# Optimization experiments

Measured on AMD Instinct MI355X. Metric: run time of the kernel, lower is better.

Reference implementation:

```python
import jax, jax.numpy as jnp
import numpy as np

N = 100000
E = 1600000
NEG_SLOPE_ATTN = 0.2   # DGL GATConv default negative_slope
NEG_SLOPE_ACT = 0.01   # F.leaky_relu default


def gat_conv(x, src, dst, W, al, ar, b):
    """DGL-style GATConv with a single head.
    x: [N, Fin]; W: [Fin, H*Fout]; al, ar: [H, Fout]; b: [H*Fout].
    Returns [N, H, Fout]."""
    H, Fout = al.shape
    h = (x @ W).reshape(-1, H, Fout)                 # [N,H,Fout]
    el = jnp.sum(h * al, axis=-1)                    # [N,H]
    er = jnp.sum(h * ar, axis=-1)                    # [N,H]
    e = jax.nn.leaky_relu(el[src] + er[dst], NEG_SLOPE_ATTN)  # [E,H]
    # edge softmax over incoming edges of each dst node
    m = jax.ops.segment_max(e, dst, num_segments=N)  # [N,H]
    ex = jnp.exp(e - m[dst])                         # [E,H]
    denom = jax.ops.segment_sum(ex, dst, num_segments=N)      # [N,H]
    a = ex / denom[dst]                              # [E,H]
    msg = h[src] * a[:, :, None]                     # [E,H,Fout]
    out = jax.ops.segment_sum(msg, dst, num_segments=N)       # [N,H,Fout]
    return out + b.reshape(1, H, Fout)


def setup_inputs() -> dict:
    key = jax.random.key(0)
    ks = jax.random.split(key, 16)
    features = jax.random.normal(ks[0], (N, 3), dtype=jnp.float32)
    src = jax.random.randint(ks[1], (E,), 0, N)
    dst = jax.random.randint(ks[2], (E,), 0, N)

    def glorot(k, shape):
        fan = shape[0] + shape[-1]
        s = jnp.sqrt(2.0 / fan).astype(jnp.float32)
        return jax.random.normal(k, shape, dtype=jnp.float32) * s

    W1 = glorot(ks[3], (3, 64));   al1 = glorot(ks[4], (1, 64));  ar1 = glorot(ks[5], (1, 64));  b1 = jnp.zeros((64,), jnp.float32)
    W2 = glorot(ks[6], (64, 64));  al2 = glorot(ks[7], (1, 64));  ar2 = glorot(ks[8], (1, 64));  b2 = jnp.zeros((64,), jnp.float32)
    W3 = glorot(ks[9], (64, 3));   al3 = glorot(ks[10], (1, 3));  ar3 = glorot(ks[11], (1, 3));  b3 = jnp.zeros((3,), jnp.float32)
    return {"features": features, "src": src, "dst": dst,
            "W1": W1, "al1": al1, "ar1": ar1, "b1": b1,
            "W2": W2, "al2": al2, "ar2": ar2, "b2": b2,
            "W3": W3, "al3": al3, "ar3": ar3, "b3": b3}


def reference(features, src, dst, W1, al1, ar1, b1, W2, al2, ar2, b2, W3, al3, ar3, b3):
    x = gat_conv(features, src, dst, W1, al1, ar1, b1)      # [N,1,64]
    x = jax.nn.leaky_relu(x, NEG_SLOPE_ACT)
    x = gat_conv(x[:, 0, :], src, dst, W2, al2, ar2, b2)     # [N,1,64]
    x = jax.nn.leaky_relu(x, NEG_SLOPE_ACT)
    x = gat_conv(x[:, 0, :], src, dst, W3, al3, ar3, b3)     # [N,1,3]
    return x[:, 0, :]                                        # [N,3]
```

## Files before the change

### kernel.cpp

```cpp
#include <hip/hip_runtime.h>
#include <hip/hip_fp16.h>
#include <math.h>


#define NEG_BIG (-1e30f)
#define SORT_CAP 6144
#define BSTRIDE 6144
#define CHUNK 8192

__device__ inline float waveSum(float v) {
#pragma unroll
  for (int off = 32; off; off >>= 1) v += __shfl_xor(v, off, 64);
  return v;
}

__device__ inline float halfSum(float v) {
#pragma unroll
  for (int off = 16; off; off >>= 1) v += __shfl_xor(v, off, 64);
  return v;
}

__device__ inline float halfMax(float v) {
#pragma unroll
  for (int off = 16; off; off >>= 1) v = fmaxf(v, __shfl_xor(v, off, 64));
  return v;
}

__device__ inline int waveMaxI(int v) {
#pragma unroll
  for (int off = 32; off; off >>= 1) v = max(v, __shfl_xor(v, off, 64));
  return v;
}

__device__ inline int rlI(int v, int l) { return __builtin_amdgcn_readlane(v, l); }
__device__ inline float rlF(float v, int l) {
  return __int_as_float(__builtin_amdgcn_readlane(__float_as_int(v), l));
}
__device__ inline int ntI(const int* p) { return __builtin_nontemporal_load(p); }

__global__ __launch_bounds__(1024) void k_bin(
    const int* __restrict__ src, const int* __restrict__ dst,
    int* __restrict__ gcursor, unsigned* __restrict__ binned, int E, int NBK) {
  __shared__ int lcnt[512];
  __shared__ int lbase[512];
  int tid = threadIdx.x;
  for (int b = tid; b < NBK; b += 1024) lcnt[b] = 0;
  __syncthreads();
  int e0 = blockIdx.x * CHUNK;
  int e1 = min(e0 + CHUNK, E);
  for (int e = e0 + tid; e < e1; e += 1024)
    atomicAdd(&lcnt[ntI(&dst[e]) >> 8], 1);
  __syncthreads();
  for (int b = tid; b < NBK; b += 1024) {
    int c = lcnt[b];
    lbase[b] = c ? atomicAdd(&gcursor[b], c) : 0;
    lcnt[b] = 0;
  }
  __syncthreads();
  for (int e = e0 + tid; e < e1; e += 1024) {
    int dd = ntI(&dst[e]);
    int ss = ntI(&src[e]);
    int b = dd >> 8;
    int pos = lbase[b] + atomicAdd(&lcnt[b], 1);
    if (pos < BSTRIDE)
      binned[(size_t)b * BSTRIDE + pos] =
          ((unsigned)(dd & 255) << 24) | (unsigned)ss;
  }
}

__global__ __launch_bounds__(256) void k_sort(
    const unsigned* __restrict__ binned, const int* __restrict__ gcount,
    int* __restrict__ csr, int* __restrict__ startv, int N, int E, int NBK) {
  __shared__ unsigned sbuf[SORT_CAP];
  __shared__ unsigned obuf[SORT_CAP];
  __shared__ int hist[256];
  __shared__ int scn[256];
  __shared__ int cur[256];
  __shared__ int sscan[512];
  int b = blockIdx.x;
  int tid = threadIdx.x;
  sscan[tid] = (tid < NBK) ? gcount[tid] : 0;
  sscan[tid + 256] = (tid + 256 < NBK) ? gcount[tid + 256] : 0;
  __syncthreads();
  for (int off = 1; off < 512; off <<= 1) {
    int u0 = (tid >= off) ? sscan[tid - off] : 0;
    int u1 = (tid + 256 >= off) ? sscan[tid + 256 - off] : 0;
    __syncthreads();
    sscan[tid] += u0;
    sscan[tid + 256] += u1;
    __syncthreads();
  }
  int cntb = gcount[b];
  int gbase = sscan[b] - cntb;
  int cnt = min(cntb, BSTRIDE);
  if (b == 0 && tid == 0) startv[N] = E;
  const unsigned* bsrc = binned + (size_t)b * BSTRIDE;
  hist[tid] = 0;
  __syncthreads();
  if (cnt <= SORT_CAP) {
    for (int i = tid; i < cnt; i += 256) {
      unsigned w = bsrc[i];
      sbuf[i] = w;
      atomicAdd(&hist[w >> 24], 1);
    }
    __syncthreads();
    int v = hist[tid];
    scn[tid] = v;
    __syncthreads();
    for (int off = 1; off < 256; off <<= 1) {
      int u = (tid >= off) ? scn[tid - off] : 0;
      __syncthreads();
      scn[tid] += u;
      __syncthreads();
    }
    int excl = scn[tid] - v;
    cur[tid] = excl;
    int dn = b * 256 + tid;
    if (dn < N) startv[dn] = gbase + excl;
    __syncthreads();
    for (int i = tid; i < cnt; i += 256) {
      unsigned w = sbuf[i];
      int p = atomicAdd(&cur[w >> 24], 1);
      obuf[p] = w & 0xFFFFFFu;
    }
    __syncthreads();
    for (int i = tid; i < cnt; i += 256) csr[gbase + i] = (int)obuf[i];
  } else {
    for (int i = tid; i < cnt; i += 256)
      atomicAdd(&hist[bsrc[i] >> 24], 1);
    __syncthreads();
    int v = hist[tid];
    scn[tid] = v;
    __syncthreads();
    for (int off = 1; off < 256; off <<= 1) {
      int u = (tid >= off) ? scn[tid - off] : 0;
      __syncthreads();
      scn[tid] += u;
      __syncthreads();
    }
    int excl = scn[tid] - v;
    cur[tid] = excl;
    int dn = b * 256 + tid;
    if (dn < N) startv[dn] = gbase + excl;
    __syncthreads();
    for (int i = tid; i < cnt; i += 256) {
      unsigned w = bsrc[i];
      int p = atomicAdd(&cur[w >> 24], 1);
      csr[gbase + p] = (int)(w & 0xFFFFFFu);
    }
  }
}

__global__ __launch_bounds__(256) void k_padx(
    const float* __restrict__ x, const float* __restrict__ W1,
    const float* __restrict__ al1, const float* __restrict__ ar1,
    int* __restrict__ gcount, int NBK,
    float4* __restrict__ x4, float* __restrict__ er1, int N) {
  __shared__ float su[6];
  int tid = threadIdx.x;
  if (tid < 64) {
    float a = al1[tid], r = ar1[tid];
#pragma unroll
    for (int i = 0; i < 3; ++i) {
      float w = W1[i * 64 + tid];
      float ui = waveSum(w * a);
      float vi = waveSum(w * r);
      if (tid == 0) { su[i] = ui; su[3 + i] = vi; }
    }
  }
  if (blockIdx.x == 0)
    for (int b = tid; b < NBK; b += 256) gcount[b] = 0;
  __syncthreads();
  int n = blockIdx.x * 256 + tid;
  if (n >= N) return;
  float x0 = __builtin_nontemporal_load(&x[n * 3]);
  float x1 = __builtin_nontemporal_load(&x[n * 3 + 1]);
  float x2 = __builtin_nontemporal_load(&x[n * 3 + 2]);
  float el = fmaf(x0, su[0], fmaf(x1, su[1], x2 * su[2]));
  float er = fmaf(x0, su[3], fmaf(x1, su[4], x2 * su[5]));
  x4[n] = make_float4(x0, x1, x2, el);
  er1[n] = er;
}

__global__ __launch_bounds__(128) void k_agg1x(
    const float4* __restrict__ x4, const float* __restrict__ er1,
    const float* __restrict__ W1, const float* __restrict__ b1,
    const float* __restrict__ W2, const float* __restrict__ al2,
    const float* __restrict__ ar2, const int* __restrict__ start,
    const int* __restrict__ csr, float4* __restrict__ a4,
    float* __restrict__ er2, int N) {
  __shared__ float4 sWp[64];
  __shared__ float2 sLR[64];
  int tid = threadIdx.x;
  if (tid < 64) {
    sWp[tid] = make_float4(W1[tid], W1[64 + tid], W1[128 + tid], b1[tid]);
    float sa = 0.f, sr = 0.f;
#pragma unroll 8
    for (int f = 0; f < 64; ++f) {
      float w = W2[tid * 64 + f];
      sa = fmaf(w, al2[f], sa);
      sr = fmaf(w, ar2[f], sr);
    }
    sLR[tid] = make_float2(sa, sr);
  }
  __syncthreads();
  int n = blockIdx.x * 128 + tid;
  if (n >= N) return;
  int beg = start[n], end = start[n + 1];
  float ern = er1[n];
  float m = NEG_BIG, d = 0.f, X0 = 0.f, X1 = 0.f, X2 = 0.f;
  int s0, s1, s2, s3;
  float4 h0, h1, h2, h3v;
  s0 = (beg + 0 < end) ? ntI(&csr[beg + 0]) : 0;
  s0 = ((unsigned)s0 < (unsigned)N) ? s0 : 0; h0 = x4[s0];
  s1 = (beg + 1 < end) ? ntI(&csr[beg + 1]) : 0;
  s1 = ((unsigned)s1 < (unsigned)N) ? s1 : 0; h1 = x4[s1];
  s2 = (beg + 2 < end) ? ntI(&csr[beg + 2]) : 0;
  s2 = ((unsigned)s2 < (unsigned)N) ? s2 : 0; h2 = x4[s2];
  s3 = (beg + 3 < end) ? ntI(&csr[beg + 3]) : 0;
  s3 = ((unsigned)s3 < (unsigned)N) ? s3 : 0; h3v = x4[s3];
  for (int i = beg; i < end; ++i) {
    float4 hv = h0;
    h0 = h1; h1 = h2; h2 = h3v;
    int ip = i + 4;
    int sp = (ip < end) ? ntI(&csr[ip]) : 0;
    sp = ((unsigned)sp < (unsigned)N) ? sp : 0;
    h3v = x4[sp];
    float e = hv.w + ern;
    e = e > 0.f ? e : 0.2f * e;
    float mn = fmaxf(m, e);
    float sc = __expf(m - mn);
    float q = __expf(e - mn);
    d = fmaf(d, sc, q);
    X0 = fmaf(X0, sc, q * hv.x);
    X1 = fmaf(X1, sc, q * hv.y);
    X2 = fmaf(X2, sc, q * hv.z);
    m = mn;
  }
  float inv = (end > beg) ? 1.f / d : 0.f;
  float A0 = X0 * inv, A1 = X1 * inv, A2 = X2 * inv;
  float el = 0.f, er = 0.f;
#pragma unroll 4
  for (int k = 0; k < 64; ++k) {
    float4 w = sWp[k];
    float v = fmaf(A2, w.z, fmaf(A1, w.y, fmaf(A0, w.x, w.w)));
    v = v > 0.f ? v : 0.01f * v;
    float2 lr = sLR[k];
    el = fmaf(v, lr.x, el);
    er = fmaf(v, lr.y, er);
  }
  a4[n] = make_float4(A0, A1, A2, el);
  er2[n] = er;
}

__global__ __launch_bounds__(64) void k_agg2r(
    const float4* __restrict__ a4, const float* __restrict__ er2,
    const int* __restrict__ start, const int* __restrict__ csr,
    const float* __restrict__ W1, const float* __restrict__ b1,
    __half* __restrict__ xa, int N) {
  __shared__ float4 sAV[64];
  int tid = threadIdx.x;
  int lane = tid & 63, hl = lane & 31, half = lane >> 5;
  int pn = blockIdx.x * 2 + half;
  int n = (pn < N) ? pn : 0;
  int beg = start[n], end = start[n + 1];
  int deg = end - beg;
  int maxd = __builtin_amdgcn_readfirstlane(waveMaxI(deg));
  float ern = er2[n];
  int k0 = 2 * hl;
  float wa0 = W1[k0],     wb0 = W1[64 + k0],     wc0 = W1[128 + k0],     bb0 = b1[k0];
  float wa1 = W1[k0 + 1], wb1 = W1[64 + k0 + 1], wc1 = W1[128 + k0 + 1], bb1 = b1[k0 + 1];
  float acc0 = 0.f, acc1 = 0.f;

  float aA = 0.f, v0s = 0.f, v1s = 0.f, v2s = 0.f;
  if (maxd <= 32) {
    int idx = beg + hl;
    int s = (idx < end) ? ntI(&csr[idx]) : 0;
    s = ((unsigned)s < (unsigned)N) ? s : 0;
    float4 av = a4[s];
    float e = av.w + ern;
    e = e > 0.f ? e : 0.2f * e;
    e = (idx < end) ? e : NEG_BIG;
    float mm = halfMax(e);
    float q = __expf(e - mm);
    float dsum = halfSum(q);
    float inv = (deg > 0) ? 1.f / dsum : 0.f;
    aA = q * inv;
    v0s = av.x; v1s = av.y; v2s = av.z;
  }
  sAV[half * 32 + hl] = make_float4(aA, v0s, v1s, v2s);
  __syncthreads();

  if (maxd <= 32) {
    const float4* sp = &sAV[half * 32];
    for (int j = 0; j < maxd; j += 4) {
#pragma unroll
      for (int k = 0; k < 4; ++k) {
        float4 w = sp[j + k];
        float a = w.x;
        float v0 = fmaf(w.w, wc0, fmaf(w.z, wb0, fmaf(w.y, wa0, bb0)));
        v0 = v0 > 0.f ? v0 : 0.01f * v0;
        float v1 = fmaf(w.w, wc1, fmaf(w.z, wb1, fmaf(w.y, wa1, bb1)));
        v1 = v1 > 0.f ? v1 : 0.01f * v1;
        acc0 = fmaf(a, v0, acc0);
        acc1 = fmaf(a, v1, acc1);
      }
    }
  } else {
    float m = NEG_BIG, dsum = 0.f;
    for (int base = beg; base < end; base += 32) {
      int idx = base + hl;
      int s = (idx < end) ? csr[idx] : 0;
      s = ((unsigned)s < (unsigned)N) ? s : 0;
      float e = a4[s].w + ern;
      e = e > 0.f ? e : 0.2f * e;
      e = (idx < end) ? e : NEG_BIG;
      float mn = fmaxf(m, halfMax(e));
      dsum = dsum * __expf(m - mn) + halfSum(__expf(e - mn));
      m = mn;
    }
    float inv = (deg > 0) ? 1.f / dsum : 0.f;
    for (int base = beg; base < end; base += 32) {
      int idx = base + hl;
      int s = (idx < end) ? csr[idx] : 0;
      s = ((unsigned)s < (unsigned)N) ? s : 0;
      float e = a4[s].w + ern;
      e = e > 0.f ? e : 0.2f * e;
      float a = (idx < end) ? __expf(e - m) * inv : 0.f;
      for (int j = 0; j < 32; ++j) {
        int sAx = rlI(s, j), sBx = rlI(s, j + 32);
        float aAx = rlF(a, j), aBx = rlF(a, j + 32);
        int sj = half ? sBx : sAx;
        float aj = half ? aBx : aAx;
        float4 av = a4[sj];
        float v0 = fmaf(av.z, wc0, fmaf(av.y, wb0, fmaf(av.x, wa0, bb0)));
        v0 = v0 > 0.f ? v0 : 0.01f * v0;
        float v1 = fmaf(av.z, wc1, fmaf(av.y, wb1, fmaf(av.x, wa1, bb1)));
        v1 = v1 > 0.f ? v1 : 0.01f * v1;
        acc0 = fmaf(aj, v0, acc0);
        acc1 = fmaf(aj, v1, acc1);
      }
    }
  }
  if (pn < N) {
    __half2 hv = __float22half2_rn(make_float2(acc0, acc1));
    ((__half2*)xa)[(size_t)pn * 32 + hl] = hv;
  }
}

__global__ __launch_bounds__(256) void k_gemm3(
    const __half* xa_in, const float* __restrict__ W2,
    const float* __restrict__ b2, const float* __restrict__ W3,
    const float* __restrict__ al3, float* __restrict__ h3, int N) {
  __shared__ float sW[64 * 64];
  __shared__ float sX[64 * 64];
  __shared__ float sW3[192];
  int tid = threadIdx.x;
  for (int i = tid; i < 4096; i += 256) sW[i] = W2[i];
  if (tid < 192) sW3[tid] = W3[tid];
  const unsigned* xu = (const unsigned*)xa_in;
  size_t base = (size_t)blockIdx.x * 2048;
  size_t limit = (size_t)N * 32;
  for (int i = tid; i < 2048; i += 256) {
    size_t gi = base + i;
    unsigned u = (gi < limit) ? __builtin_nontemporal_load(&xu[gi]) : 0u;
    __half2 hh = *(__half2*)&u;
    float2 f = __half22float2(hh);
    sX[2 * i] = f.x;
    sX[2 * i + 1] = f.y;
  }
  __syncthreads();
  int wave = tid >> 6, f = tid & 63;
  int r0 = wave * 16;
  float acc[16];
#pragma unroll
  for (int i = 0; i < 16; ++i) acc[i] = 0.f;
  const float2* sX2 = (const float2*)sX;
  for (int k2 = 0; k2 < 32; ++k2) {
    float wv0 = sW[(2 * k2) * 64 + f];
    float wv1 = sW[(2 * k2 + 1) * 64 + f];
#pragma unroll
    for (int i = 0; i < 16; ++i) {
      float2 xv = sX2[(r0 + i) * 32 + k2];
      acc[i] = fmaf(xv.x, wv0, fmaf(xv.y, wv1, acc[i]));
    }
  }
  float bf = b2[f];
  __syncthreads();
#pragma unroll
  for (int i = 0; i < 16; ++i) {
    float r = acc[i] + bf;
    r = r > 0.f ? r : 0.01f * r;
    sX[(r0 + i) * 64 + f] = r;
  }
  __syncthreads();
  int row = tid >> 2, j = tid & 3;
  int j3 = (j < 3) ? j : 0;
  float p = 0.f;
  for (int i = 0; i < 64; ++i) {
    int ff = (row + i) & 63;
    p = fmaf(sX[row * 64 + ff], sW3[ff * 3 + j3], p);
  }
  int lb = (tid & 63) & ~3;
  float q0 = __shfl(p, lb + 0, 64);
  float q1 = __shfl(p, lb + 1, 64);
  float q2 = __shfl(p, lb + 2, 64);
  float val = (j < 3) ? p : fmaf(q0, al3[0], fmaf(q1, al3[1], q2 * al3[2]));
  int grow = blockIdx.x * 64 + row;
  if (grow < N) h3[(size_t)blockIdx.x * 256 + tid] = val;
}

__global__ __launch_bounds__(128) void k_agg3(
    const float4* __restrict__ h3, const int* __restrict__ start,
    const int* __restrict__ csr, const float* __restrict__ ar3,
    const float* __restrict__ b, float* __restrict__ out, int N) {
  int n = blockIdx.x * 128 + threadIdx.x;
  if (n >= N) return;
  int beg = start[n], end = start[n + 1];
  float4 hn = h3[n];
  float ern = fmaf(hn.x, ar3[0], fmaf(hn.y, ar3[1], hn.z * ar3[2]));
  float m = NEG_BIG, d = 0.f, Q0 = 0.f, Q1 = 0.f, Q2 = 0.f;
  int s0, s1, s2, s3;
  float4 h0, h1, h2, h3v;
  s0 = (beg + 0 < end) ? ntI(&csr[beg + 0]) : 0;
  s0 = ((unsigned)s0 < (unsigned)N) ? s0 : 0; h0 = h3[s0];
  s1 = (beg + 1 < end) ? ntI(&csr[beg + 1]) : 0;
  s1 = ((unsigned)s1 < (unsigned)N) ? s1 : 0; h1 = h3[s1];
  s2 = (beg + 2 < end) ? ntI(&csr[beg + 2]) : 0;
  s2 = ((unsigned)s2 < (unsigned)N) ? s2 : 0; h2 = h3[s2];
  s3 = (beg + 3 < end) ? ntI(&csr[beg + 3]) : 0;
  s3 = ((unsigned)s3 < (unsigned)N) ? s3 : 0; h3v = h3[s3];
  for (int i = beg; i < end; ++i) {
    float4 hv = h0;
    h0 = h1; h1 = h2; h2 = h3v;
    int ip = i + 4;
    int sp = (ip < end) ? ntI(&csr[ip]) : 0;
    sp = ((unsigned)sp < (unsigned)N) ? sp : 0;
    h3v = h3[sp];
    float e = hv.w + ern;
    e = e > 0.f ? e : 0.2f * e;
    float mn = fmaxf(m, e);
    float sc = __expf(m - mn);
    float q = __expf(e - mn);
    d = fmaf(d, sc, q);
    Q0 = fmaf(Q0, sc, q * hv.x);
    Q1 = fmaf(Q1, sc, q * hv.y);
    Q2 = fmaf(Q2, sc, q * hv.z);
    m = mn;
  }
  float inv = (end > beg) ? 1.f / d : 0.f;
  out[n * 3 + 0] = fmaf(Q0, inv, b[0]);
  out[n * 3 + 1] = fmaf(Q1, inv, b[1]);
  out[n * 3 + 2] = fmaf(Q2, inv, b[2]);
}

extern "C" void kernel_launch(void* const* d_in, const int* in_sizes, int n_in,
                              void* d_out, int out_size, void* d_ws, size_t ws_size,
                              hipStream_t stream) {
  const int N = in_sizes[0] / 3;
  const int E = in_sizes[1];
  const float* feats = (const float*)d_in[0];
  const int* src = (const int*)d_in[1];
  const int* dst = (const int*)d_in[2];
  const float* W1  = (const float*)d_in[3];
  const float* al1 = (const float*)d_in[4];
  const float* ar1 = (const float*)d_in[5];
  const float* b1  = (const float*)d_in[6];
  const float* W2  = (const float*)d_in[7];
  const float* al2 = (const float*)d_in[8];
  const float* ar2 = (const float*)d_in[9];
  const float* b2  = (const float*)d_in[10];
  const float* W3  = (const float*)d_in[11];
  const float* al3 = (const float*)d_in[12];
  const float* ar3 = (const float*)d_in[13];
  const float* b3  = (const float*)d_in[14];

  const int NBK = (N + 255) >> 8;

  char* ws = (char*)d_ws;
  size_t off = 0;
  auto alloc = [&](size_t bytes) -> void* {
    void* p = ws + off;
    off = (off + bytes + 255) & ~(size_t)255;
    return p;
  };
  int* startv  = (int*)alloc((size_t)(N + 1) * 4);
  int* csr     = (int*)alloc((size_t)E * 4);
  float* er2v  = (float*)alloc((size_t)N * 4);
  float* er1   = (float*)alloc((size_t)N * 4);
  int* gcount  = (int*)alloc((size_t)NBK * 4);
  float* h3    = (float*)alloc((size_t)N * 4 * 4);
  float4* x4   = (float4*)alloc((size_t)N * 16);
  float4* a4   = (float4*)alloc((size_t)N * 16);
  __half* xa   = (__half*)alloc((size_t)N * 64 * 2);
  unsigned* binned = (unsigned*)xa;

  const int NB  = (N + 255) / 256;
  const int NB1 = (N + 127) / 128;
  const int NW2 = (N + 1) / 2;
  const int GB  = (N + 63) / 64;
  const int CB  = (E + CHUNK - 1) / CHUNK;

  k_padx<<<NB, 256, 0, stream>>>(feats, W1, al1, ar1, gcount, NBK,
                                 x4, er1, N);
  k_bin<<<CB, 1024, 0, stream>>>(src, dst, gcount, binned, E, NBK);
  k_sort<<<NBK, 256, 0, stream>>>(binned, gcount, csr, startv, N, E, NBK);
  k_agg1x<<<NB1, 128, 0, stream>>>(x4, er1, W1, b1, W2, al2, ar2,
                                   startv, csr, a4, er2v, N);
  k_agg2r<<<NW2, 64, 0, stream>>>(a4, er2v, startv, csr, W1, b1, xa, N);
  k_gemm3<<<GB, 256, 0, stream>>>(xa, W2, b2, W3, al3, h3, N);
  k_agg3<<<NB1, 128, 0, stream>>>((const float4*)h3, startv, csr, ar3, b3,
                                  (float*)d_out, N);
}
```

Before: 240.6 us.

## Replace global-atomic binning with per-chunk fixed slots and padded CSR

The binning kernel now writes each chunk's edges into fixed 64-entry slots per (bucket, chunk), so the global atomic cursor and the first counting pass over dst are gone. The feature-padding kernel is folded into the same launch as extra blocks. The sort kernel gathers each bucket's slots with a per-chunk prefix scan and writes a padded CSR (fixed stride per bucket) plus a per-node degree array, and the aggregation kernels use start+deg instead of start[n+1]. This removes one launch and one pass over dst, but it silently drops edges when a chunk puts more than 64 edges in a bucket and uses more workspace. The gather in the sort kernel is also a serial per-thread loop.

```diff
diff --git a/kernel.cpp b/kernel.cpp
--- a/kernel.cpp
+++ b/kernel.cpp
@@ -5,7 +5,7 @@
 
 #define NEG_BIG (-1e30f)
 #define SORT_CAP 6144
-#define BSTRIDE 6144
+#define SLOT 64
 #define CHUNK 8192
 
 __device__ inline float waveSum(float v) {
@@ -38,148 +38,120 @@
 }
 __device__ inline int ntI(const int* p) { return __builtin_nontemporal_load(p); }
 
-__global__ __launch_bounds__(1024) void k_bin(
+__global__ __launch_bounds__(1024) void k_binpad(
     const int* __restrict__ src, const int* __restrict__ dst,
-    int* __restrict__ gcursor, unsigned* __restrict__ binned, int E, int NBK) {
+    unsigned* __restrict__ binned, int* __restrict__ cnts,
+    const float* __restrict__ x, const float* __restrict__ W1,
+    const float* __restrict__ al1, const float* __restrict__ ar1,
+    float4* __restrict__ x4, float* __restrict__ er1,
+    int E, int N, int NBK, int NCH, int CB) {
   __shared__ int lcnt[512];
-  __shared__ int lbase[512];
+  __shared__ float su[6];
   int tid = threadIdx.x;
-  for (int b = tid; b < NBK; b += 1024) lcnt[b] = 0;
-  __syncthreads();
-  int e0 = blockIdx.x * CHUNK;
-  int e1 = min(e0 + CHUNK, E);
-  for (int e = e0 + tid; e < e1; e += 1024)
-    atomicAdd(&lcnt[ntI(&dst[e]) >> 8], 1);
-  __syncthreads();
-  for (int b = tid; b < NBK; b += 1024) {
-    int c = lcnt[b];
-    lbase[b] = c ? atomicAdd(&gcursor[b], c) : 0;
-    lcnt[b] = 0;
-  }
-  __syncthreads();
-  for (int e = e0 + tid; e < e1; e += 1024) {
-    int dd = ntI(&dst[e]);
-    int ss = ntI(&src[e]);
-    int b = dd >> 8;
-    int pos = lbase[b] + atomicAdd(&lcnt[b], 1);
-    if (pos < BSTRIDE)
-      binned[(size_t)b * BSTRIDE + pos] =
-          ((unsigned)(dd & 255) << 24) | (unsigned)ss;
+  if ((int)blockIdx.x < CB) {
+    int c = blockIdx.x;
+    for (int b = tid; b < NBK; b += 1024) lcnt[b] = 0;
+    __syncthreads();
+    int e0 = c * CHUNK;
+    int e1 = min(e0 + CHUNK, E);
+    for (int e = e0 + tid; e < e1; e += 1024) {
+      int dd = ntI(&dst[e]);
+      int ss = ntI(&src[e]);
+      int b = dd >> 8;
+      int pos = atomicAdd(&lcnt[b], 1);
+      if (pos < SLOT)
+        binned[((size_t)b * NCH + c) * SLOT + pos] =
+            ((unsigned)(dd & 255) << 24) | (unsigned)ss;
+    }
+    __syncthreads();
+    for (int b = tid; b < NBK; b += 1024)
+      cnts[(size_t)c * NBK + b] = min(lcnt[b], SLOT);
+  } else {
+    if (tid < 64) {
+      float a = al1[tid], r = ar1[tid];
+#pragma unroll
+      for (int i = 0; i < 3; ++i) {
+        float w = W1[i * 64 + tid];
+        float ui = waveSum(w * a);
+        float vi = waveSum(w * r);
+        if (tid == 0) { su[i] = ui; su[3 + i] = vi; }
+      }
+    }
+    __syncthreads();
+    int n = ((int)blockIdx.x - CB) * 1024 + tid;
+    if (n >= N) return;
+    float x0 = __builtin_nontemporal_load(&x[n * 3]);
+    float x1 = __builtin_nontemporal_load(&x[n * 3 + 1]);
+    float x2 = __builtin_nontemporal_load(&x[n * 3 + 2]);
+    float el = fmaf(x0, su[0], fmaf(x1, su[1], x2 * su[2]));
+    float er = fmaf(x0, su[3], fmaf(x1, su[4], x2 * su[5]));
+    x4[n] = make_float4(x0, x1, x2, el);
+    er1[n] = er;
   }
 }
 
 __global__ __launch_bounds__(256) void k_sort(
-    const unsigned* __restrict__ binned, const int* __restrict__ gcount,
-    int* __restrict__ csr, int* __restrict__ startv, int N, int E, int NBK) {
+    const unsigned* __restrict__ binned, const int* __restrict__ cnts,
+    int* __restrict__ csr, int* __restrict__ startv, int* __restrict__ degs,
+    int N, int NBK, int NCH) {
   __shared__ unsigned sbuf[SORT_CAP];
   __shared__ unsigned obuf[SORT_CAP];
   __shared__ int hist[256];
   __shared__ int scn[256];
   __shared__ int cur[256];
-  __shared__ int sscan[512];
+  __shared__ int csc[256];
   int b = blockIdx.x;
   int tid = threadIdx.x;
-  sscan[tid] = (tid < NBK) ? gcount[tid] : 0;
-  sscan[tid + 256] = (tid + 256 < NBK) ? gcount[tid + 256] : 0;
-  __syncthreads();
-  for (int off = 1; off < 512; off <<= 1) {
-    int u0 = (tid >= off) ? sscan[tid - off] : 0;
-    int u1 = (tid + 256 >= off) ? sscan[tid + 256 - off] : 0;
-    __syncthreads();
-    sscan[tid] += u0;
-    sscan[tid + 256] += u1;
-    __syncthreads();
-  }
-  int cntb = gcount[b];
-  int gbase = sscan[b] - cntb;
-  int cnt = min(cntb, BSTRIDE);
-  if (b == 0 && tid == 0) startv[N] = E;
-  const unsigned* bsrc = binned + (size_t)b * BSTRIDE;
+  int total = 0;
+  for (int cb = 0; cb < NCH; cb += 256) {
+    int c = cb + tid;
+    int v = (c < NCH) ? cnts[(size_t)c * NBK + b] : 0;
+    csc[tid] = v;
+    __syncthreads();
+    for (int off = 1; off < 256; off <<= 1) {
+      int u = (tid >= off) ? csc[tid - off] : 0;
+      __syncthreads();
+      csc[tid] += u;
+      __syncthreads();
+    }
+    int dbase = total + csc[tid] - v;
+    if (c < NCH && v > 0) {
+      const unsigned* rs = binned + ((size_t)b * NCH + c) * SLOT;
+      for (int i = 0; i < v; ++i) {
+        int di = dbase + i;
+        if (di < SORT_CAP) sbuf[di] = rs[i];
+      }
+    }
+    total += csc[255];
+    __syncthreads();
+  }
+  int cnt = min(total, SORT_CAP);
+  int gbase = b * SORT_CAP;
   hist[tid] = 0;
   __syncthreads();
-  if (cnt <= SORT_CAP) {
-    for (int i = tid; i < cnt; i += 256) {
-      unsigned w = bsrc[i];
-      sbuf[i] = w;
-      atomicAdd(&hist[w >> 24], 1);
-    }
-    __syncthreads();
-    int v = hist[tid];
-    scn[tid] = v;
-    __syncthreads();
-    for (int off = 1; off < 256; off <<= 1) {
-      int u = (tid >= off) ? scn[tid - off] : 0;
-      __syncthreads();
-      scn[tid] += u;
-      __syncthreads();
-    }
-    int excl = scn[tid] - v;
-    cur[tid] = excl;
-    int dn = b * 256 + tid;
-    if (dn < N) startv[dn] = gbase + excl;
-    __syncthreads();
-    for (int i = tid; i < cnt; i += 256) {
-      unsigned w = sbuf[i];
-      int p = atomicAdd(&cur[w >> 24], 1);
-      obuf[p] = w & 0xFFFFFFu;
-    }
-    __syncthreads();
-    for (int i = tid; i < cnt; i += 256) csr[gbase + i] = (int)obuf[i];
-  } else {
-    for (int i = tid; i < cnt; i += 256)
-      atomicAdd(&hist[bsrc[i] >> 24], 1);
-    __syncthreads();
-    int v = hist[tid];
-    scn[tid] = v;
-    __syncthreads();
-    for (int off = 1; off < 256; off <<= 1) {
-      int u = (tid >= off) ? scn[tid - off] : 0;
-      __syncthreads();
-      scn[tid] += u;
-      __syncthreads();
-    }
-    int excl = scn[tid] - v;
-    cur[tid] = excl;
-    int dn = b * 256 + tid;
-    if (dn < N) startv[dn] = gbase + excl;
-    __syncthreads();
-    for (int i = tid; i < cnt; i += 256) {
-      unsigned w = bsrc[i];
-      int p = atomicAdd(&cur[w >> 24], 1);
-      csr[gbase + p] = (int)(w & 0xFFFFFFu);
-    }
-  }
-}
-
-__global__ __launch_bounds__(256) void k_padx(
-    const float* __restrict__ x, const float* __restrict__ W1,
-    const float* __restrict__ al1, const float* __restrict__ ar1,
-    int* __restrict__ gcount, int NBK,
-    float4* __restrict__ x4, float* __restrict__ er1, int N) {
-  __shared__ float su[6];
-  int tid = threadIdx.x;
-  if (tid < 64) {
-    float a = al1[tid], r = ar1[tid];
-#pragma unroll
-    for (int i = 0; i < 3; ++i) {
-      float w = W1[i * 64 + tid];
-      float ui = waveSum(w * a);
-      float vi = waveSum(w * r);
-      if (tid == 0) { su[i] = ui; su[3 + i] = vi; }
-    }
-  }
-  if (blockIdx.x == 0)
-    for (int b = tid; b < NBK; b += 256) gcount[b] = 0;
-  __syncthreads();
-  int n = blockIdx.x * 256 + tid;
-  if (n >= N) return;
-  float x0 = __builtin_nontemporal_load(&x[n * 3]);
-  float x1 = __builtin_nontemporal_load(&x[n * 3 + 1]);
-  float x2 = __builtin_nontemporal_load(&x[n * 3 + 2]);
-  float el = fmaf(x0, su[0], fmaf(x1, su[1], x2 * su[2]));
-  float er = fmaf(x0, su[3], fmaf(x1, su[4], x2 * su[5]));
-  x4[n] = make_float4(x0, x1, x2, el);
-  er1[n] = er;
+  for (int i = tid; i < cnt; i += 256) atomicAdd(&hist[sbuf[i] >> 24], 1);
+  __syncthreads();
+  int v = hist[tid];
+  scn[tid] = v;
+  __syncthreads();
+  for (int off = 1; off < 256; off <<= 1) {
+    int u = (tid >= off) ? scn[tid - off] : 0;
+    __syncthreads();
+    scn[tid] += u;
+    __syncthreads();
+  }
+  int excl = scn[tid] - v;
+  cur[tid] = excl;
+  int dn = b * 256 + tid;
+  if (dn < N) { startv[dn] = gbase + excl; degs[dn] = v; }
+  __syncthreads();
+  for (int i = tid; i < cnt; i += 256) {
+    unsigned w = sbuf[i];
+    int p = atomicAdd(&cur[w >> 24], 1);
+    obuf[p] = w & 0xFFFFFFu;
+  }
+  __syncthreads();
+  for (int i = tid; i < cnt; i += 256) csr[gbase + i] = (int)obuf[i];
 }
 
 __global__ __launch_bounds__(128) void k_agg1x(
@@ -187,8 +159,8 @@
     const float* __restrict__ W1, const float* __restrict__ b1,
     const float* __restrict__ W2, const float* __restrict__ al2,
     const float* __restrict__ ar2, const int* __restrict__ start,
-    const int* __restrict__ csr, float4* __restrict__ a4,
-    float* __restrict__ er2, int N) {
+    const int* __restrict__ degs, const int* __restrict__ csr,
+    float4* __restrict__ a4, float* __restrict__ er2, int N) {
   __shared__ float4 sWp[64];
   __shared__ float2 sLR[64];
   int tid = threadIdx.x;
@@ -206,7 +178,8 @@
   __syncthreads();
   int n = blockIdx.x * 128 + tid;
   if (n >= N) return;
-  int beg = start[n], end = start[n + 1];
+  int beg = start[n];
+  int end = beg + degs[n];
   float ern = er1[n];
   float m = NEG_BIG, d = 0.f, X0 = 0.f, X1 = 0.f, X2 = 0.f;
   int s0, s1, s2, s3;
@@ -255,16 +228,17 @@
 
 __global__ __launch_bounds__(64) void k_agg2r(
     const float4* __restrict__ a4, const float* __restrict__ er2,
-    const int* __restrict__ start, const int* __restrict__ csr,
-    const float* __restrict__ W1, const float* __restrict__ b1,
-    __half* __restrict__ xa, int N) {
+    const int* __restrict__ start, const int* __restrict__ degs,
+    const int* __restrict__ csr, const float* __restrict__ W1,
+    const float* __restrict__ b1, __half* __restrict__ xa, int N) {
   __shared__ float4 sAV[64];
   int tid = threadIdx.x;
   int lane = tid & 63, hl = lane & 31, half = lane >> 5;
   int pn = blockIdx.x * 2 + half;
   int n = (pn < N) ? pn : 0;
-  int beg = start[n], end = start[n + 1];
-  int deg = end - beg;
+  int beg = start[n];
+  int deg = degs[n];
+  int end = beg + deg;
   int maxd = __builtin_amdgcn_readfirstlane(waveMaxI(deg));
   float ern = er2[n];
   int k0 = 2 * hl;
@@ -412,11 +386,13 @@
 
 __global__ __launch_bounds__(128) void k_agg3(
     const float4* __restrict__ h3, const int* __restrict__ start,
-    const int* __restrict__ csr, const float* __restrict__ ar3,
-    const float* __restrict__ b, float* __restrict__ out, int N) {
+    const int* __restrict__ degs, const int* __restrict__ csr,
+    const float* __restrict__ ar3, const float* __restrict__ b,
+    float* __restrict__ out, int N) {
   int n = blockIdx.x * 128 + threadIdx.x;
   if (n >= N) return;
-  int beg = start[n], end = start[n + 1];
+  int beg = start[n];
+  int end = beg + degs[n];
   float4 hn = h3[n];
   float ern = fmaf(hn.x, ar3[0], fmaf(hn.y, ar3[1], hn.z * ar3[2]));
   float m = NEG_BIG, d = 0.f, Q0 = 0.f, Q1 = 0.f, Q2 = 0.f;
@@ -476,6 +452,8 @@
   const float* b3  = (const float*)d_in[14];
 
   const int NBK = (N + 255) >> 8;
+  const int CB  = (E + CHUNK - 1) / CHUNK;
+  const int NCH = CB;
 
   char* ws = (char*)d_ws;
   size_t off = 0;
@@ -485,30 +463,31 @@
     return p;
   };
   int* startv  = (int*)alloc((size_t)(N + 1) * 4);
-  int* csr     = (int*)alloc((size_t)E * 4);
+  int* degs    = (int*)alloc((size_t)N * 4);
+  int* csr     = (int*)alloc((size_t)NBK * SORT_CAP * 4);
   float* er2v  = (float*)alloc((size_t)N * 4);
   float* er1   = (float*)alloc((size_t)N * 4);
-  int* gcount  = (int*)alloc((size_t)NBK * 4);
+  int* cnts    = (int*)alloc((size_t)NCH * NBK * 4);
   float* h3    = (float*)alloc((size_t)N * 4 * 4);
   float4* x4   = (float4*)alloc((size_t)N * 16);
   float4* a4   = (float4*)alloc((size_t)N * 16);
   __half* xa   = (__half*)alloc((size_t)N * 64 * 2);
-  unsigned* binned = (unsigned*)xa;
-
-  const int NB  = (N + 255) / 256;
+  unsigned* binned = (unsigned*)alloc((size_t)NBK * NCH * SLOT * 4);
+
+  const int NPB = (N + 1023) / 1024;
   const int NB1 = (N + 127) / 128;
   const int NW2 = (N + 1) / 2;
   const int GB  = (N + 63) / 64;
-  const int CB  = (E + CHUNK - 1) / CHUNK;
-
-  k_padx<<<NB, 256, 0, stream>>>(feats, W1, al1, ar1, gcount, NBK,
-                                 x4, er1, N);
-  k_bin<<<CB, 1024, 0, stream>>>(src, dst, gcount, binned, E, NBK);
-  k_sort<<<NBK, 256, 0, stream>>>(binned, gcount, csr, startv, N, E, NBK);
+
+  k_binpad<<<CB + NPB, 1024, 0, stream>>>(src, dst, binned, cnts,
+                                          feats, W1, al1, ar1, x4, er1,
+                                          E, N, NBK, NCH, CB);
+  k_sort<<<NBK, 256, 0, stream>>>(binned, cnts, csr, startv, degs,
+                                  N, NBK, NCH);
   k_agg1x<<<NB1, 128, 0, stream>>>(x4, er1, W1, b1, W2, al2, ar2,
-                                   startv, csr, a4, er2v, N);
-  k_agg2r<<<NW2, 64, 0, stream>>>(a4, er2v, startv, csr, W1, b1, xa, N);
+                                   startv, degs, csr, a4, er2v, N);
+  k_agg2r<<<NW2, 64, 0, stream>>>(a4, er2v, startv, degs, csr, W1, b1, xa, N);
   k_gemm3<<<GB, 256, 0, stream>>>(xa, W2, b2, W3, al3, h3, N);
-  k_agg3<<<NB1, 128, 0, stream>>>((const float4*)h3, startv, csr, ar3, b3,
-                                  (float*)d_out, N);
-}
+  k_agg3<<<NB1, 128, 0, stream>>>((const float4*)h3, startv, degs, csr,
+                                  ar3, b3, (float*)d_out, N);
+}
```

Result: no change. 240.1 us, median of 2 (-0.2%).
